# Kernel tuning notes

Measured on AMD Instinct MI355X. Metric: run time of the kernel, lower is better.

The kernel has to match this reference:

```python
import jax, jax.numpy as jnp
import numpy as np

NEG_SLOPE = 0.2

def setup_inputs() -> dict:
    key = jax.random.key(0)
    k1, k2, k3 = jax.random.split(key, 3)
    N, d, attn = 1024, 256, 256
    H = jax.random.normal(k1, (N, d), dtype=jnp.float32)
    # nn.Linear(2*d, attn, bias=False).weight has shape [attn, 2*d]
    W = jax.random.normal(k2, (attn, 2 * d), dtype=jnp.float32) * 0.05
    a = jax.random.normal(k3, (attn, 1), dtype=jnp.float32) * 0.05
    return {"H": H, "W": W, "a": a}

def reference(H, W, a):
    # Faithful to: E = leakyrelu(Linear(cat[H_i, H_j])); scores = E @ a; alpha = softmax(scores, dim=1); out = alpha @ H
    # Decompose W into halves acting on H_i and H_j to avoid the N x N x 2d concat:
    d = H.shape[1]
    W1, W2 = W[:, :d], W[:, d:]          # each [attn, d]
    Wh1 = H @ W1.T                        # [N, attn] (contribution of H_i)
    Wh2 = H @ W2.T                        # [N, attn] (contribution of H_j)
    E = jax.nn.leaky_relu(Wh1[:, None, :] + Wh2[None, :, :], NEG_SLOPE)  # [N, N, attn]
    scores = jnp.einsum('ijk,ko->ij', E, a)   # [N, N]
    alpha = jax.nn.softmax(scores, axis=1)    # softmax over j (dim=1)
    return alpha @ H                          # [N, d] weighted sum of H_j
```

## Files before the change

kernel.cpp:

```cpp
#include <hip/hip_runtime.h>


#define HALF 524288
#define LDW 68

#define FENCE_BAR() do {                                   \
    __builtin_amdgcn_sched_barrier(0);                     \
    asm volatile("s_waitcnt lgkmcnt(0)" ::: "memory");     \
    __builtin_amdgcn_s_barrier();                          \
    __builtin_amdgcn_sched_barrier(0);                     \
} while (0)

#define BAR_ONLY() do {                                    \
    __builtin_amdgcn_sched_barrier(0);                     \
    asm volatile("s_waitcnt lgkmcnt(0)" ::: "memory");     \
    __builtin_amdgcn_s_barrier();                          \
    __builtin_amdgcn_sched_barrier(0);                     \
} while (0)

__global__ __launch_bounds__(256) void k1_gemm_wh(const float* __restrict__ H,
                                                  const float* __restrict__ W,
                                                  float* __restrict__ Whp) {
    __shared__ float As[64][36];
    __shared__ float Bs[32][36];
    const int bi = blockIdx.x, bm = blockIdx.y, bz = blockIdx.z;
    const int t = threadIdx.x;
    const int ti = t >> 4, tj = t & 15;
    const int i0 = ti * 4;
    const int half = bm >> 3;
    const int kbase = bz * 128;
    float acc[4][2] = {};
    for (int kc = 0; kc < 128; kc += 32) {
        const int kg = kbase + kc;
        {
            const int r = t >> 2, c = (t & 3) * 8;
            *(float4*)&As[r][c] = *(const float4*)&H[(bi * 64 + r) * 256 + kg + c];
            *(float4*)&As[r][c + 4] =
                *(const float4*)&H[(bi * 64 + r) * 256 + kg + c + 4];
        }
        {
            const int r = t >> 3, c = (t & 7) * 4;
            const int wrow = (bm * 32 + r) & 255;
            *(float4*)&Bs[r][c] =
                *(const float4*)&W[wrow * 512 + half * 256 + kg + c];
        }
        __syncthreads();
#pragma unroll
        for (int k = 0; k < 32; k += 4) {
            float4 a[4], b[2];
#pragma unroll
            for (int r = 0; r < 4; ++r) a[r] = *(const float4*)&As[i0 + r][k];
#pragma unroll
            for (int c = 0; c < 2; ++c) b[c] = *(const float4*)&Bs[tj + 16 * c][k];
#pragma unroll
            for (int r = 0; r < 4; ++r)
#pragma unroll
                for (int c = 0; c < 2; ++c) {
                    acc[r][c] = fmaf(a[r].x, b[c].x, acc[r][c]);
                    acc[r][c] = fmaf(a[r].y, b[c].y, acc[r][c]);
                    acc[r][c] = fmaf(a[r].z, b[c].z, acc[r][c]);
                    acc[r][c] = fmaf(a[r].w, b[c].w, acc[r][c]);
                }
        }
        __syncthreads();
    }
    float* dst = Whp + (size_t)bz * HALF;
#pragma unroll
    for (int r = 0; r < 4; ++r)
#pragma unroll
        for (int c = 0; c < 2; ++c)
            dst[(size_t)(bi * 64 + i0 + r) * 512 + bm * 32 + tj + 16 * c] = acc[r][c];
}

__global__ __launch_bounds__(256) void kW_merge(const float* __restrict__ Whp,
                                                const float* __restrict__ a,
                                                float* __restrict__ Wh,
                                                float* __restrict__ s2) {
    const int t = threadIdx.x;
    const int row = blockIdx.x * 2 + (t >> 7);
    const int col = (t & 127) * 4;
    const size_t off = (size_t)row * 512 + col;
    float4 v0 = *(const float4*)&Whp[off];
    float4 v1 = *(const float4*)&Whp[HALF + off];
    float4 v = make_float4(v0.x + v1.x, v0.y + v1.y, v0.z + v1.z, v0.w + v1.w);
    *(float4*)&Wh[off] = v;
    if (col >= 256) {
        float4 av = *(const float4*)&a[col - 256];
        float p = av.x * v.x + av.y * v.y + av.z * v.z + av.w * v.w;
#pragma unroll
        for (int o = 32; o > 0; o >>= 1) p += __shfl_xor(p, o);
        if ((t & 63) == 0) s2[row] = 0.6f * p;
    }
}

__global__ __launch_bounds__(256) void kF_flash(const float* __restrict__ Wh,
                                                const float* __restrict__ a,
                                                const float* __restrict__ s2,
                                                const float* __restrict__ H,
                                                float* __restrict__ avp,
                                                float* __restrict__ mbuf,
                                                float* __restrict__ lbuf) {
    __shared__ float X1[2][32][LDW];
    __shared__ float X2[2][64][LDW];
    __shared__ float P[32][LDW];
    __shared__ float bsh[256];
    const int bi = blockIdx.x, bj = blockIdx.y;
    const int t = threadIdx.x;
    const int ti = t >> 4, tj = t & 15;
    const int i0 = ti * 2;
    const int r1 = t >> 3, c1 = (t & 7) * 8;
    const int r2 = t >> 2, c2 = (t & 3) * 16;
    const float* g1 = Wh + (size_t)(bi * 32 + r1) * 512 + c1;
    const float* g2 = Wh + (size_t)(bj * 64 + r2) * 512 + 256 + c2;
    const float* gH = H + (size_t)(bj * 64 + r2) * 256 + c2;

    float4 A0, A1, A2, A3, A4, A5, B0, B1, B2, B3, B4, B5;

#define LOADC_A(mc) do { A0 = *(const float4*)(g1 + (mc)*64); \
    A1 = *(const float4*)(g1 + (mc)*64 + 4);                  \
    A2 = *(const float4*)(g2 + (mc)*64);                      \
    A3 = *(const float4*)(g2 + (mc)*64 + 4);                  \
    A4 = *(const float4*)(g2 + (mc)*64 + 8);                  \
    A5 = *(const float4*)(g2 + (mc)*64 + 12); } while (0)
#define LOADC_B(mc) do { B0 = *(const float4*)(g1 + (mc)*64); \
    B1 = *(const float4*)(g1 + (mc)*64 + 4);                  \
    B2 = *(const float4*)(g2 + (mc)*64);                      \
    B3 = *(const float4*)(g2 + (mc)*64 + 4);                  \
    B4 = *(const float4*)(g2 + (mc)*64 + 8);                  \
    B5 = *(const float4*)(g2 + (mc)*64 + 12); } while (0)
#define WRITEC_A(buf) do { *(float4*)&X1[buf][r1][c1] = A0;   \
    *(float4*)&X1[buf][r1][c1 + 4] = A1;                      \
    *(float4*)&X2[buf][r2][c2] = A2;                          \
    *(float4*)&X2[buf][r2][c2 + 4] = A3;                      \
    *(float4*)&X2[buf][r2][c2 + 8] = A4;                      \
    *(float4*)&X2[buf][r2][c2 + 12] = A5; } while (0)
#define WRITEC_B(buf) do { *(float4*)&X1[buf][r1][c1] = B0;   \
    *(float4*)&X1[buf][r1][c1 + 4] = B1;                      \
    *(float4*)&X2[buf][r2][c2] = B2;                          \
    *(float4*)&X2[buf][r2][c2 + 4] = B3;                      \
    *(float4*)&X2[buf][r2][c2 + 8] = B4;                      \
    *(float4*)&X2[buf][r2][c2 + 12] = B5; } while (0)

    LOADC_A(0);
    float s2v0 = s2[bj * 64 + tj];
    float s2v1 = s2[bj * 64 + tj + 16];
    float s2v2 = s2[bj * 64 + tj + 32];
    float s2v3 = s2[bj * 64 + tj + 48];
    if (t < 64) {
        float4 av = *(const float4*)&a[t * 4];
        *(float4*)&bsh[t * 4] =
            make_float4(0.4f * av.x, 0.4f * av.y, 0.4f * av.z, 0.4f * av.w);
    }

    float acc[2][4] = {};
#pragma unroll
    for (int mc = 0; mc < 4; ++mc) {
        const int buf = mc & 1;
        if (mc < 3) {
            if (buf == 0) LOADC_B(mc + 1); else LOADC_A(mc + 1);
        }
        if (buf == 0) WRITEC_A(0); else WRITEC_B(1);
        FENCE_BAR();
#pragma unroll
        for (int k = 0; k < 64; k += 4) {
            float4 x1[2], x2[4];
#pragma unroll
            for (int r = 0; r < 2; ++r) x1[r] = *(const float4*)&X1[buf][i0 + r][k];
#pragma unroll
            for (int c = 0; c < 4; ++c)
                x2[c] = *(const float4*)&X2[buf][tj + 16 * c][k];
            const float4 bv = *(const float4*)&bsh[mc * 64 + k];
#pragma unroll
            for (int r = 0; r < 2; ++r)
#pragma unroll
                for (int c = 0; c < 4; ++c) {
                    acc[r][c] = fmaf(fabsf(x1[r].x + x2[c].x), bv.x, acc[r][c]);
                    acc[r][c] = fmaf(fabsf(x1[r].y + x2[c].y), bv.y, acc[r][c]);
                    acc[r][c] = fmaf(fabsf(x1[r].z + x2[c].z), bv.z, acc[r][c]);
                    acc[r][c] = fmaf(fabsf(x1[r].w + x2[c].w), bv.w, acc[r][c]);
                }
        }
        BAR_ONLY();
    }

    acc[0][0] += s2v0; acc[1][0] += s2v0;
    acc[0][1] += s2v1; acc[1][1] += s2v1;
    acc[0][2] += s2v2; acc[1][2] += s2v2;
    acc[0][3] += s2v3; acc[1][3] += s2v3;

    A2 = *(const float4*)(gH);
    A3 = *(const float4*)(gH + 4);
    A4 = *(const float4*)(gH + 8);
    A5 = *(const float4*)(gH + 12);

    float mm0, mm1, l00, l01;
#pragma unroll
    for (int r = 0; r < 2; ++r) {
        float mm = fmaxf(fmaxf(acc[r][0], acc[r][1]), fmaxf(acc[r][2], acc[r][3]));
        mm = fmaxf(mm, __shfl_xor(mm, 1));
        mm = fmaxf(mm, __shfl_xor(mm, 2));
        mm = fmaxf(mm, __shfl_xor(mm, 4));
        mm = fmaxf(mm, __shfl_xor(mm, 8));
        float l0 = 0.f;
#pragma unroll
        for (int c = 0; c < 4; ++c) {
            acc[r][c] = __expf(acc[r][c] - mm);
            l0 += acc[r][c];
        }
        l0 += __shfl_xor(l0, 1);
        l0 += __shfl_xor(l0, 2);
        l0 += __shfl_xor(l0, 4);
        l0 += __shfl_xor(l0, 8);
#pragma unroll
        for (int c = 0; c < 4; ++c) P[i0 + r][tj + 16 * c] = acc[r][c];
        if (r == 0) { mm0 = mm; l00 = l0; } else { mm1 = mm; l01 = l0; }
    }
    FENCE_BAR();

#pragma unroll
    for (int cc = 0; cc < 4; ++cc) {
        const int buf = cc & 1;
        if (cc < 3) {
            if (buf == 0) {
                B2 = *(const float4*)(gH + (cc + 1) * 64);
                B3 = *(const float4*)(gH + (cc + 1) * 64 + 4);
                B4 = *(const float4*)(gH + (cc + 1) * 64 + 8);
                B5 = *(const float4*)(gH + (cc + 1) * 64 + 12);
            } else {
                A2 = *(const float4*)(gH + (cc + 1) * 64);
                A3 = *(const float4*)(gH + (cc + 1) * 64 + 4);
                A4 = *(const float4*)(gH + (cc + 1) * 64 + 8);
                A5 = *(const float4*)(gH + (cc + 1) * 64 + 12);
            }
        }
        if (buf == 0) {
            *(float4*)&X2[0][r2][c2] = A2;
            *(float4*)&X2[0][r2][c2 + 4] = A3;
            *(float4*)&X2[0][r2][c2 + 8] = A4;
            *(float4*)&X2[0][r2][c2 + 12] = A5;
        } else {
            *(float4*)&X2[1][r2][c2] = B2;
            *(float4*)&X2[1][r2][c2 + 4] = B3;
            *(float4*)&X2[1][r2][c2 + 8] = B4;
            *(float4*)&X2[1][r2][c2 + 12] = B5;
        }
        FENCE_BAR();
        float acc2[2][4] = {};
#pragma unroll
        for (int jj = 0; jj < 64; jj += 4) {
            float4 pv[2], h[4];
#pragma unroll
            for (int r = 0; r < 2; ++r) pv[r] = *(const float4*)&P[i0 + r][jj];
#pragma unroll
            for (int q = 0; q < 4; ++q)
                h[q] = *(const float4*)&X2[buf][jj + q][tj * 4];
#pragma unroll
            for (int r = 0; r < 2; ++r) {
                acc2[r][0] = fmaf(pv[r].x, h[0].x, acc2[r][0]);
                acc2[r][1] = fmaf(pv[r].x, h[0].y, acc2[r][1]);
                acc2[r][2] = fmaf(pv[r].x, h[0].z, acc2[r][2]);
                acc2[r][3] = fmaf(pv[r].x, h[0].w, acc2[r][3]);
                acc2[r][0] = fmaf(pv[r].y, h[1].x, acc2[r][0]);
                acc2[r][1] = fmaf(pv[r].y, h[1].y, acc2[r][1]);
                acc2[r][2] = fmaf(pv[r].y, h[1].z, acc2[r][2]);
                acc2[r][3] = fmaf(pv[r].y, h[1].w, acc2[r][3]);
                acc2[r][0] = fmaf(pv[r].z, h[2].x, acc2[r][0]);
                acc2[r][1] = fmaf(pv[r].z, h[2].y, acc2[r][1]);
                acc2[r][2] = fmaf(pv[r].z, h[2].z, acc2[r][2]);
                acc2[r][3] = fmaf(pv[r].z, h[2].w, acc2[r][3]);
                acc2[r][0] = fmaf(pv[r].w, h[3].x, acc2[r][0]);
                acc2[r][1] = fmaf(pv[r].w, h[3].y, acc2[r][1]);
                acc2[r][2] = fmaf(pv[r].w, h[3].z, acc2[r][2]);
                acc2[r][3] = fmaf(pv[r].w, h[3].w, acc2[r][3]);
            }
        }
#pragma unroll
        for (int r = 0; r < 2; ++r) {
            *(float4*)&avp[(size_t)bj * 262144 + (size_t)(bi * 32 + i0 + r) * 256 +
                           cc * 64 + tj * 4] =
                make_float4(acc2[r][0], acc2[r][1], acc2[r][2], acc2[r][3]);
        }
        BAR_ONLY();
    }
    if (tj == 0) {
        const int gi = bi * 32 + i0;
        mbuf[bj * 1024 + gi] = mm0;
        lbuf[bj * 1024 + gi] = l00;
        mbuf[bj * 1024 + gi + 1] = mm1;
        lbuf[bj * 1024 + gi + 1] = l01;
    }
#undef LOADC_A
#undef LOADC_B
#undef WRITEC_A
#undef WRITEC_B
}

__global__ __launch_bounds__(256) void kM_merge(const float* __restrict__ avp,
                                                const float* __restrict__ mbuf,
                                                const float* __restrict__ lbuf,
                                                float* __restrict__ out) {
    const int t = threadIdx.x;
    const int i = blockIdx.x * 4 + (t >> 6);
    const int c0 = (t & 63) * 4;
    float ms[16], es[16];
    float M = -1e30f;
#pragma unroll
    for (int s = 0; s < 16; ++s) {
        ms[s] = mbuf[s * 1024 + i];
        M = fmaxf(M, ms[s]);
    }
    float L = 0.f;
#pragma unroll
    for (int s = 0; s < 16; ++s) {
        es[s] = __expf(ms[s] - M);
        L = fmaf(es[s], lbuf[s * 1024 + i], L);
    }
    const float inv = 1.0f / L;
    float4 o = make_float4(0.f, 0.f, 0.f, 0.f);
#pragma unroll
    for (int s = 0; s < 16; ++s) {
        float4 p = *(const float4*)&avp[(size_t)s * 262144 + (size_t)i * 256 + c0];
        o.x = fmaf(es[s], p.x, o.x);
        o.y = fmaf(es[s], p.y, o.y);
        o.z = fmaf(es[s], p.z, o.z);
        o.w = fmaf(es[s], p.w, o.w);
    }
    o.x *= inv; o.y *= inv; o.z *= inv; o.w *= inv;
    *(float4*)&out[(size_t)i * 256 + c0] = o;
}

extern "C" void kernel_launch(void* const* d_in, const int* in_sizes, int n_in,
                              void* d_out, int out_size, void* d_ws, size_t ws_size,
                              hipStream_t stream) {
    const float* H = (const float*)d_in[0];
    const float* W = (const float*)d_in[1];
    const float* a = (const float*)d_in[2];
    float* out = (float*)d_out;
    float* ws = (float*)d_ws;

    float* avp = ws;
    float* Whp = ws;
    float* Wh = ws + (4u << 20);
    float* mbuf = Wh + HALF;
    float* lbuf = mbuf + 16384;
    float* s2 = lbuf + 16384;

    hipLaunchKernelGGL(k1_gemm_wh, dim3(16, 16, 2), dim3(256), 0, stream, H, W, Whp);
    hipLaunchKernelGGL(kW_merge, dim3(512), dim3(256), 0, stream, Whp, a, Wh, s2);
    hipLaunchKernelGGL(kF_flash, dim3(32, 16), dim3(256), 0, stream, Wh, a, s2, H,
                       avp, mbuf, lbuf);
    hipLaunchKernelGGL(kM_merge, dim3(256), dim3(256), 0, stream, avp, mbuf, lbuf, out);
}
```

Measured before the change: 50.18 us.

## Stage full H tile in shared memory and compute P·H in one pass

The P·H phase previously streamed H in four 64-column chunks through a double buffer, with a barrier per chunk and a 2x4 register tile per thread. It now loads the whole 64x256 H tile into a shared buffer aliased over the X1/X2 staging area, then runs a single pass where each thread computes a 4x8 output tile. This removes three barrier rounds and raises arithmetic intensity per shared-memory load. In exchange, shared memory per block grows and register pressure rises, which could reduce occupancy, and the H load is no longer overlapped with compute.

```diff
diff --git a/kernel.cpp b/kernel.cpp
--- a/kernel.cpp
+++ b/kernel.cpp
@@ -2,16 +2,8 @@
 
 
 #define HALF 524288
-#define LDW 68
 
 #define FENCE_BAR() do {                                   \
-    __builtin_amdgcn_sched_barrier(0);                     \
-    asm volatile("s_waitcnt lgkmcnt(0)" ::: "memory");     \
-    __builtin_amdgcn_s_barrier();                          \
-    __builtin_amdgcn_sched_barrier(0);                     \
-} while (0)
-
-#define BAR_ONLY() do {                                    \
     __builtin_amdgcn_sched_barrier(0);                     \
     asm volatile("s_waitcnt lgkmcnt(0)" ::: "memory");     \
     __builtin_amdgcn_s_barrier();                          \
@@ -100,10 +92,12 @@
                                                 float* __restrict__ avp,
                                                 float* __restrict__ mbuf,
                                                 float* __restrict__ lbuf) {
-    __shared__ float X1[2][32][LDW];
-    __shared__ float X2[2][64][LDW];
-    __shared__ float P[32][LDW];
+    __shared__ float SH[16640];
+    __shared__ float P[32 * 68];
     __shared__ float bsh[256];
+    float* X1 = SH;
+    float* X2 = SH + 4352;
+    float* Hs = SH;
     const int bi = blockIdx.x, bj = blockIdx.y;
     const int t = threadIdx.x;
     const int ti = t >> 4, tj = t & 15;
@@ -112,7 +106,8 @@
     const int r2 = t >> 2, c2 = (t & 3) * 16;
     const float* g1 = Wh + (size_t)(bi * 32 + r1) * 512 + c1;
     const float* g2 = Wh + (size_t)(bj * 64 + r2) * 512 + 256 + c2;
-    const float* gH = H + (size_t)(bj * 64 + r2) * 256 + c2;
+    const int hr = t >> 2, hc = (t & 3) * 64;
+    const float* gH = H + (size_t)(bj * 64 + hr) * 256 + hc;
 
     float4 A0, A1, A2, A3, A4, A5, B0, B1, B2, B3, B4, B5;
 
@@ -128,18 +123,20 @@
     B3 = *(const float4*)(g2 + (mc)*64 + 4);                  \
     B4 = *(const float4*)(g2 + (mc)*64 + 8);                  \
     B5 = *(const float4*)(g2 + (mc)*64 + 12); } while (0)
-#define WRITEC_A(buf) do { *(float4*)&X1[buf][r1][c1] = A0;   \
-    *(float4*)&X1[buf][r1][c1 + 4] = A1;                      \
-    *(float4*)&X2[buf][r2][c2] = A2;                          \
-    *(float4*)&X2[buf][r2][c2 + 4] = A3;                      \
-    *(float4*)&X2[buf][r2][c2 + 8] = A4;                      \
-    *(float4*)&X2[buf][r2][c2 + 12] = A5; } while (0)
-#define WRITEC_B(buf) do { *(float4*)&X1[buf][r1][c1] = B0;   \
-    *(float4*)&X1[buf][r1][c1 + 4] = B1;                      \
-    *(float4*)&X2[buf][r2][c2] = B2;                          \
-    *(float4*)&X2[buf][r2][c2 + 4] = B3;                      \
-    *(float4*)&X2[buf][r2][c2 + 8] = B4;                      \
-    *(float4*)&X2[buf][r2][c2 + 12] = B5; } while (0)
+#define WRITEC_A(buf) do {                                    \
+    *(float4*)&X1[((buf) * 32 + r1) * 68 + c1] = A0;          \
+    *(float4*)&X1[((buf) * 32 + r1) * 68 + c1 + 4] = A1;      \
+    *(float4*)&X2[((buf) * 64 + r2) * 68 + c2] = A2;          \
+    *(float4*)&X2[((buf) * 64 + r2) * 68 + c2 + 4] = A3;      \
+    *(float4*)&X2[((buf) * 64 + r2) * 68 + c2 + 8] = A4;      \
+    *(float4*)&X2[((buf) * 64 + r2) * 68 + c2 + 12] = A5; } while (0)
+#define WRITEC_B(buf) do {                                    \
+    *(float4*)&X1[((buf) * 32 + r1) * 68 + c1] = B0;          \
+    *(float4*)&X1[((buf) * 32 + r1) * 68 + c1 + 4] = B1;      \
+    *(float4*)&X2[((buf) * 64 + r2) * 68 + c2] = B2;          \
+    *(float4*)&X2[((buf) * 64 + r2) * 68 + c2 + 4] = B3;      \
+    *(float4*)&X2[((buf) * 64 + r2) * 68 + c2 + 8] = B4;      \
+    *(float4*)&X2[((buf) * 64 + r2) * 68 + c2 + 12] = B5; } while (0)
 
     LOADC_A(0);
     float s2v0 = s2[bj * 64 + tj];
@@ -165,10 +162,11 @@
         for (int k = 0; k < 64; k += 4) {
             float4 x1[2], x2[4];
 #pragma unroll
-            for (int r = 0; r < 2; ++r) x1[r] = *(const float4*)&X1[buf][i0 + r][k];
+            for (int r = 0; r < 2; ++r)
+                x1[r] = *(const float4*)&X1[(buf * 32 + i0 + r) * 68 + k];
 #pragma unroll
             for (int c = 0; c < 4; ++c)
-                x2[c] = *(const float4*)&X2[buf][tj + 16 * c][k];
+                x2[c] = *(const float4*)&X2[(buf * 64 + tj + 16 * c) * 68 + k];
             const float4 bv = *(const float4*)&bsh[mc * 64 + k];
 #pragma unroll
             for (int r = 0; r < 2; ++r)
@@ -180,7 +178,7 @@
                     acc[r][c] = fmaf(fabsf(x1[r].w + x2[c].w), bv.w, acc[r][c]);
                 }
         }
-        BAR_ONLY();
+        FENCE_BAR();
     }
 
     acc[0][0] += s2v0; acc[1][0] += s2v0;
@@ -188,10 +186,14 @@
     acc[0][2] += s2v2; acc[1][2] += s2v2;
     acc[0][3] += s2v3; acc[1][3] += s2v3;
 
-    A2 = *(const float4*)(gH);
-    A3 = *(const float4*)(gH + 4);
-    A4 = *(const float4*)(gH + 8);
-    A5 = *(const float4*)(gH + 12);
+    float4 h0 = *(const float4*)(gH);
+    float4 h1 = *(const float4*)(gH + 4);
+    float4 h2 = *(const float4*)(gH + 8);
+    float4 h3 = *(const float4*)(gH + 12);
+    float4 h4 = *(const float4*)(gH + 16);
+    float4 h5 = *(const float4*)(gH + 20);
+    float4 h6 = *(const float4*)(gH + 24);
+    float4 h7 = *(const float4*)(gH + 28);
 
     float mm0, mm1, l00, l01;
 #pragma unroll
@@ -212,75 +214,70 @@
         l0 += __shfl_xor(l0, 4);
         l0 += __shfl_xor(l0, 8);
 #pragma unroll
-        for (int c = 0; c < 4; ++c) P[i0 + r][tj + 16 * c] = acc[r][c];
+        for (int c = 0; c < 4; ++c) P[(i0 + r) * 68 + tj + 16 * c] = acc[r][c];
         if (r == 0) { mm0 = mm; l00 = l0; } else { mm1 = mm; l01 = l0; }
     }
     FENCE_BAR();
 
-#pragma unroll
-    for (int cc = 0; cc < 4; ++cc) {
-        const int buf = cc & 1;
-        if (cc < 3) {
-            if (buf == 0) {
-                B2 = *(const float4*)(gH + (cc + 1) * 64);
-                B3 = *(const float4*)(gH + (cc + 1) * 64 + 4);
-                B4 = *(const float4*)(gH + (cc + 1) * 64 + 8);
-                B5 = *(const float4*)(gH + (cc + 1) * 64 + 12);
-            } else {
-                A2 = *(const float4*)(gH + (cc + 1) * 64);
-                A3 = *(const float4*)(gH + (cc + 1) * 64 + 4);
-                A4 = *(const float4*)(gH + (cc + 1) * 64 + 8);
-                A5 = *(const float4*)(gH + (cc + 1) * 64 + 12);
+    *(float4*)&Hs[hr * 260 + hc] = h0;
+    *(float4*)&Hs[hr * 260 + hc + 4] = h1;
+    *(float4*)&Hs[hr * 260 + hc + 8] = h2;
+    *(float4*)&Hs[hr * 260 + hc + 12] = h3;
+    *(float4*)&Hs[hr * 260 + hc + 16] = h4;
+    *(float4*)&Hs[hr * 260 + hc + 20] = h5;
+    *(float4*)&Hs[hr * 260 + hc + 24] = h6;
+    *(float4*)&Hs[hr * 260 + hc + 28] = h7;
+    h0 = *(const float4*)(gH + 32);
+    h1 = *(const float4*)(gH + 36);
+    h2 = *(const float4*)(gH + 40);
+    h3 = *(const float4*)(gH + 44);
+    h4 = *(const float4*)(gH + 48);
+    h5 = *(const float4*)(gH + 52);
+    h6 = *(const float4*)(gH + 56);
+    h7 = *(const float4*)(gH + 60);
+    *(float4*)&Hs[hr * 260 + hc + 32] = h0;
+    *(float4*)&Hs[hr * 260 + hc + 36] = h1;
+    *(float4*)&Hs[hr * 260 + hc + 40] = h2;
+    *(float4*)&Hs[hr * 260 + hc + 44] = h3;
+    *(float4*)&Hs[hr * 260 + hc + 48] = h4;
+    *(float4*)&Hs[hr * 260 + hc + 52] = h5;
+    *(float4*)&Hs[hr * 260 + hc + 56] = h6;
+    *(float4*)&Hs[hr * 260 + hc + 60] = h7;
+    FENCE_BAR();
+
+    const int ti2 = t >> 5, tj2 = t & 31;
+    const int ip = ti2 * 4;
+    const int ca = tj2 * 4, cb = 128 + tj2 * 4;
+    float4 acc2[4][2] = {};
+#pragma unroll
+    for (int jj = 0; jj < 64; jj += 4) {
+        float4 pv[4];
+#pragma unroll
+        for (int r = 0; r < 4; ++r) pv[r] = *(const float4*)&P[(ip + r) * 68 + jj];
+#pragma unroll
+        for (int q = 0; q < 4; ++q) {
+            float4 ha = *(const float4*)&Hs[(jj + q) * 260 + ca];
+            float4 hb = *(const float4*)&Hs[(jj + q) * 260 + cb];
+#pragma unroll
+            for (int r = 0; r < 4; ++r) {
+                const float s = (q == 0) ? pv[r].x : (q == 1) ? pv[r].y
+                              : (q == 2) ? pv[r].z : pv[r].w;
+                acc2[r][0].x = fmaf(s, ha.x, acc2[r][0].x);
+                acc2[r][0].y = fmaf(s, ha.y, acc2[r][0].y);
+                acc2[r][0].z = fmaf(s, ha.z, acc2[r][0].z);
+                acc2[r][0].w = fmaf(s, ha.w, acc2[r][0].w);
+                acc2[r][1].x = fmaf(s, hb.x, acc2[r][1].x);
+                acc2[r][1].y = fmaf(s, hb.y, acc2[r][1].y);
+                acc2[r][1].z = fmaf(s, hb.z, acc2[r][1].z);
+                acc2[r][1].w = fmaf(s, hb.w, acc2[r][1].w);
             }
         }
-        if (buf == 0) {
-            *(float4*)&X2[0][r2][c2] = A2;
-            *(float4*)&X2[0][r2][c2 + 4] = A3;
-            *(float4*)&X2[0][r2][c2 + 8] = A4;
-            *(float4*)&X2[0][r2][c2 + 12] = A5;
-        } else {
-            *(float4*)&X2[1][r2][c2] = B2;
-            *(float4*)&X2[1][r2][c2 + 4] = B3;
-            *(float4*)&X2[1][r2][c2 + 8] = B4;
-            *(float4*)&X2[1][r2][c2 + 12] = B5;
-        }
-        FENCE_BAR();
-        float acc2[2][4] = {};
-#pragma unroll
-        for (int jj = 0; jj < 64; jj += 4) {
-            float4 pv[2], h[4];
-#pragma unroll
-            for (int r = 0; r < 2; ++r) pv[r] = *(const float4*)&P[i0 + r][jj];
-#pragma unroll
-            for (int q = 0; q < 4; ++q)
-                h[q] = *(const float4*)&X2[buf][jj + q][tj * 4];
-#pragma unroll
-            for (int r = 0; r < 2; ++r) {
-                acc2[r][0] = fmaf(pv[r].x, h[0].x, acc2[r][0]);
-                acc2[r][1] = fmaf(pv[r].x, h[0].y, acc2[r][1]);
-                acc2[r][2] = fmaf(pv[r].x, h[0].z, acc2[r][2]);
-                acc2[r][3] = fmaf(pv[r].x, h[0].w, acc2[r][3]);
-                acc2[r][0] = fmaf(pv[r].y, h[1].x, acc2[r][0]);
-                acc2[r][1] = fmaf(pv[r].y, h[1].y, acc2[r][1]);
-                acc2[r][2] = fmaf(pv[r].y, h[1].z, acc2[r][2]);
-                acc2[r][3] = fmaf(pv[r].y, h[1].w, acc2[r][3]);
-                acc2[r][0] = fmaf(pv[r].z, h[2].x, acc2[r][0]);
-                acc2[r][1] = fmaf(pv[r].z, h[2].y, acc2[r][1]);
-                acc2[r][2] = fmaf(pv[r].z, h[2].z, acc2[r][2]);
-                acc2[r][3] = fmaf(pv[r].z, h[2].w, acc2[r][3]);
-                acc2[r][0] = fmaf(pv[r].w, h[3].x, acc2[r][0]);
-                acc2[r][1] = fmaf(pv[r].w, h[3].y, acc2[r][1]);
-                acc2[r][2] = fmaf(pv[r].w, h[3].z, acc2[r][2]);
-                acc2[r][3] = fmaf(pv[r].w, h[3].w, acc2[r][3]);
-            }
-        }
-#pragma unroll
-        for (int r = 0; r < 2; ++r) {
-            *(float4*)&avp[(size_t)bj * 262144 + (size_t)(bi * 32 + i0 + r) * 256 +
-                           cc * 64 + tj * 4] =
-                make_float4(acc2[r][0], acc2[r][1], acc2[r][2], acc2[r][3]);
-        }
-        BAR_ONLY();
+    }
+#pragma unroll
+    for (int r = 0; r < 4; ++r) {
+        const size_t o = (size_t)bj * 262144 + (size_t)(bi * 32 + ip + r) * 256;
+        *(float4*)&avp[o + ca] = acc2[r][0];
+        *(float4*)&avp[o + cb] = acc2[r][1];
     }
     if (tj == 0) {
         const int gi = bi * 32 + i0;
```

Result: no change. 49.29 us (median of 3 runs) (-1.8%).
